# Kernel optimization log

Hardware: AMD Instinct MI355X
Metric: run time of the kernel (lower is better)

## Reference

```python
import jax, jax.numpy as jnp
import numpy as np

B, T, D, NH, L = 8192, 100, 44, 64, 8  # batch, seq/ode steps, obs_dim, rnn hidden, latent


def setup_inputs() -> dict:
    key = jax.random.key(0)
    ks = jax.random.split(key, 12)
    s = 0.1
    return {
        "x": jax.random.normal(ks[0], (B, T, D), jnp.float32),
        "mask": jax.random.randint(ks[1], (B, T, D), 0, 2).astype(jnp.float32),
        "epsilon": jax.random.normal(ks[2], (B, L), jnp.float32),
        "Wi2h": jax.random.normal(ks[3], (D + NH, NH), jnp.float32) * s,
        "bi2h": jnp.zeros((NH,), jnp.float32),
        "Wh2o": jax.random.normal(ks[4], (NH, 2 * L), jnp.float32) * s,
        "bh2o": jnp.zeros((2 * L,), jnp.float32),
        "Wf1": jax.random.normal(ks[5], (L, NH), jnp.float32) * s,
        "bf1": jnp.zeros((NH,), jnp.float32),
        "Wf2": jax.random.normal(ks[6], (NH, NH), jnp.float32) * s,
        "bf2": jnp.zeros((NH,), jnp.float32),
        "Wf3": jax.random.normal(ks[7], (NH, L), jnp.float32) * s,
        "bf3": jnp.zeros((L,), jnp.float32),
        "Wd1": jax.random.normal(ks[8], (L, NH), jnp.float32) * s,
        "bd1": jnp.zeros((NH,), jnp.float32),
        "Wd2": jax.random.normal(ks[9], (NH, D), jnp.float32) * s,
        "bd2": jnp.zeros((D,), jnp.float32),
    }


def reference(x, mask, epsilon, Wi2h, bi2h, Wh2o, bh2o,
              Wf1, bf1, Wf2, bf2, Wf3, bf3, Wd1, bd1, Wd2, bd2):
    masked_x = x * mask  # [B,T,D]

    # --- reverse-time recognition RNN (scan over time, reversed) ---
    def rnn_step(h, obs):
        h = jnp.tanh(jnp.concatenate([obs, h], axis=1) @ Wi2h + bi2h)
        return h, None

    xs_rev = jnp.transpose(masked_x[:, ::-1, :], (1, 0, 2))  # [T,B,D]
    h0 = jnp.zeros((x.shape[0], Wi2h.shape[1]), x.dtype)
    h_final, _ = jax.lax.scan(rnn_step, h0, xs_rev)
    out = h_final @ Wh2o + bh2o  # [B,2L]
    qz0_mean, qz0_logvar = out[:, :L], out[:, L:]

    # reparameterized latent sample
    z0 = epsilon * jnp.exp(0.5 * qz0_logvar) + qz0_mean  # [B,L]

    # --- latent ODE dynamics, fixed-step RK4 over ts = linspace(0,1,100) ---
    def f(z):
        h1 = jax.nn.elu(z @ Wf1 + bf1)
        h2 = jax.nn.elu(h1 @ Wf2 + bf2)
        return h2 @ Wf3 + bf3

    dt = jnp.asarray(1.0 / (T - 1), x.dtype)

    def rk4_step(z, _):
        k1 = f(z)
        k2 = f(z + 0.5 * dt * k1)
        k3 = f(z + 0.5 * dt * k2)
        k4 = f(z + dt * k3)
        zn = z + (dt / 6.0) * (k1 + 2.0 * k2 + 2.0 * k3 + k4)
        return zn, zn

    _, zs = jax.lax.scan(rk4_step, z0, None, length=T - 1)  # [T-1,B,L]
    pred_z = jnp.transpose(jnp.concatenate([z0[None], zs], axis=0), (1, 0, 2))  # [B,T,L]

    # --- decoder ---
    pred_x = jax.nn.relu(pred_z @ Wd1 + bd1) @ Wd2 + bd2  # [B,T,D]

    # fill observed entries back in
    updated_x = jnp.where(masked_x != 0, masked_x, pred_x)

    # --- loss ---
    noise_logvar = 2.0 * jnp.log(jnp.asarray(0.3, x.dtype))
    log2pi = jnp.log(jnp.asarray(2.0 * np.pi, x.dtype))
    logpx = (-0.5 * (log2pi + noise_logvar +
                     (x - updated_x) ** 2 / jnp.exp(noise_logvar))).sum((-1, -2))  # [B]
    kl = (-0.5 * qz0_logvar + (jnp.exp(qz0_logvar) + qz0_mean ** 2) / 2.0 - 0.5).sum(-1)  # [B]
    loss = jnp.mean(-logpx + kl)
    return loss
```

## Files before the change

kernel.cpp:

```cpp
#include <hip/hip_runtime.h>
#include <stdint.h>


constexpr int B_ = 8192, T_ = 100, D_ = 44, NH_ = 64, L_ = 8;

typedef __bf16 bf16x8 __attribute__((ext_vector_type(8)));
typedef float f32x4 __attribute__((ext_vector_type(4)));
typedef uint32_t u32x4 __attribute__((ext_vector_type(4)));
typedef uint32_t u32x2 __attribute__((ext_vector_type(2)));

__device__ __forceinline__ float fexp2(float x) { return __builtin_amdgcn_exp2f(x); }
__device__ __forceinline__ float frcp(float x) { return __builtin_amdgcn_rcpf(x); }
__device__ __forceinline__ float fexp(float x) { return fexp2(x * 1.44269504088896341f); }
__device__ __forceinline__ float tanh_f(float x) {
  float e = fexp2(x * 2.88539008177792681f);
  return 1.0f - 2.0f * frcp(e + 1.0f);
}
__device__ __forceinline__ float elu_f(float x) { return x > 0.0f ? x : (fexp(x) - 1.0f); }
__device__ __forceinline__ uint32_t f2bs(float x) {
  return (uint32_t)__builtin_bit_cast(unsigned short, (__bf16)x);
}
__device__ __forceinline__ uint32_t pk(float lo, float hi) { return f2bs(lo) | (f2bs(hi) << 16); }
__device__ __forceinline__ uint32_t sh(uint32_t v, int s) { return (uint32_t)__shfl((int)v, s, 64); }
__device__ __forceinline__ f32x4 mfma16(bf16x8 a, bf16x8 b, f32x4 c) {
  return __builtin_amdgcn_mfma_f32_16x16x32_bf16(a, b, c, 0, 0, 0);
}
__device__ __forceinline__ bf16x8 pack8(float a, float b, float c, float d,
                                        float e, float f, float g, float h) {
  u32x4 u = {pk(a, b), pk(c, d), pk(e, f), pk(g, h)};
  return __builtin_bit_cast(bf16x8, u);
}
__device__ __forceinline__ float f4get(const float4& f, int i) {
  return i == 0 ? f.x : (i == 1 ? f.y : (i == 2 ? f.z : f.w));
}

__device__ __forceinline__ void xbar() {
  asm volatile("s_waitcnt lgkmcnt(0)" ::: "memory");
  __builtin_amdgcn_s_barrier();
  asm volatile("" ::: "memory");
}

__device__ __forceinline__ void ex_write(uint32_t* ex, int c, int q, int w, f32x4 e) {
  u32x2 v = {pk(e[0], e[1]), pk(e[2], e[3])};
  *(u32x2*)(ex + 36 * c + 8 * w + 2 * q) = v;
}
__device__ __forceinline__ void ex_read(const uint32_t* ex, int c, int q, bf16x8* bh) {
#pragma unroll
  for (int ks = 0; ks < 2; ++ks) {
    u32x4 r = *(const u32x4*)(ex + 36 * c + 16 * ks + 4 * q);
    bh[ks] = __builtin_bit_cast(bf16x8, r);
  }
}

__device__ __forceinline__ bf16x8 build_bz(f32x4 z, int c, int q) {
  uint32_t p01 = pk(z[0], z[1]), p23 = pk(z[2], z[3]);
  u32x4 u = {sh(p01, c), sh(p23, c), sh(p01, c + 16), sh(p23, c + 16)};
  if (q == 1) u[0] = 0x3f80u;
  return __builtin_bit_cast(bf16x8, u);
}

__global__ __launch_bounds__(256) void fused_kernel(
    const float* __restrict__ x, const float* __restrict__ mask,
    const float* __restrict__ eps,
    const float* __restrict__ Wi2h, const float* __restrict__ bi2h,
    const float* __restrict__ Wh2o, const float* __restrict__ bh2o,
    const float* __restrict__ Wf1, const float* __restrict__ bf1,
    const float* __restrict__ Wf2, const float* __restrict__ bf2,
    const float* __restrict__ Wf3, const float* __restrict__ bf3,
    const float* __restrict__ Wd1, const float* __restrict__ bd1,
    const float* __restrict__ Wd2, const float* __restrict__ bd2,
    float* __restrict__ part) {
  const int tid = threadIdx.x;
  const int w = tid >> 6;
  const int lane = tid & 63;
  const int c = lane & 15, q = lane >> 4;
  const int r0 = blockIdx.x * 16;

  __shared__ __align__(16) uint32_t exA[576];
  __shared__ __align__(16) uint32_t exB[576];
  __shared__ __align__(16) uint32_t exC[576];
  __shared__ float redbuf[4];

  bf16x8 Ai[4];
#pragma unroll
  for (int ks = 0; ks < 4; ++ks) {
    bf16x8 f;
    const int m = 16 * w + c;
#pragma unroll
    for (int i = 0; i < 8; ++i) {
      const int k = 32 * ks + 8 * q + i;
      float v = 0.0f;
      if (k < 64) v = Wi2h[(44 + k) * 64 + m];
      else if (k < 108) v = Wi2h[(k - 64) * 64 + m];
      else if (k == 108) v = bi2h[m];
      f[i] = (__bf16)v;
    }
    Ai[ks] = f;
  }
  bf16x8 Ah2o[2];
#pragma unroll
  for (int ks = 0; ks < 2; ++ks) {
    bf16x8 f;
#pragma unroll
    for (int i = 0; i < 8; ++i) f[i] = (__bf16)Wh2o[(32 * ks + 8 * q + i) * 16 + c];
    Ah2o[ks] = f;
  }
  f32x4 bo;
#pragma unroll
  for (int r = 0; r < 4; ++r) bo[r] = bh2o[4 * q + r];

  const float* xrowbase = x + (size_t)(r0 + c) * T_ * D_;
  const float* mrowbase = mask + (size_t)(r0 + c) * T_ * D_;

  auto load_obs = [&](int t, float4& a0, float4& a1, float4& b0, float4& b1,
                      float4& ma0, float4& ma1, float4& mb0, float4& mb1) {
    const float4* xr = (const float4*)(xrowbase + (size_t)t * D_);
    const float4* mr = (const float4*)(mrowbase + (size_t)t * D_);
    a0 = xr[2 * q]; a1 = xr[2 * q + 1]; ma0 = mr[2 * q]; ma1 = mr[2 * q + 1];
    float4 zz = {0.f, 0.f, 0.f, 0.f};
    b0 = zz; b1 = zz; mb0 = zz; mb1 = zz;
    if (q == 0) { b0 = xr[8]; b1 = xr[9]; mb0 = mr[8]; mb1 = mr[9]; }
    else if (q == 1) { b0 = xr[10]; mb0 = mr[10]; }
  };

  f32x4 hc = {0.f, 0.f, 0.f, 0.f};
  float4 a0, a1, b0, b1, ma0, ma1, mb0, mb1;
  load_obs(T_ - 1, a0, a1, b0, b1, ma0, ma1, mb0, mb1);

#pragma unroll 1
  for (int s = 0; s < T_; ++s) {
    uint32_t* ex = (s & 1) ? exB : exA;
    ex_write(ex, c, q, w, hc);

    const int t = T_ - 1 - s;
    float4 ca0 = a0, ca1 = a1, cb0 = b0, cb1 = b1;
    float4 cm0 = ma0, cm1 = ma1, cn0 = mb0, cn1 = mb1;
    if (t > 0) load_obs(t - 1, a0, a1, b0, b1, ma0, ma1, mb0, mb1);

    bf16x8 o2 = pack8(ca0.x * cm0.x, ca0.y * cm0.y, ca0.z * cm0.z, ca0.w * cm0.w,
                      ca1.x * cm1.x, ca1.y * cm1.y, ca1.z * cm1.z, ca1.w * cm1.w);
    const float e44 = (q == 1) ? 1.0f : cb1.x * cn1.x;
    bf16x8 o3 = pack8(cb0.x * cn0.x, cb0.y * cn0.y, cb0.z * cn0.z, cb0.w * cn0.w,
                      e44, cb1.y * cn1.y, cb1.z * cn1.z, cb1.w * cn1.w);

    xbar();
    bf16x8 bh[2];
    ex_read(ex, c, q, bh);

    f32x4 zero = {0.f, 0.f, 0.f, 0.f};
    f32x4 acc = mfma16(Ai[0], bh[0], zero);
    acc = mfma16(Ai[1], bh[1], acc);
    acc = mfma16(Ai[2], o2, acc);
    acc = mfma16(Ai[3], o3, acc);
#pragma unroll
    for (int r = 0; r < 4; ++r) hc[r] = tanh_f(acc[r]);
  }

  ex_write(exA, c, q, w, hc);
  xbar();
  bf16x8 bhF[2];
  ex_read(exA, c, q, bhF);
  f32x4 o = mfma16(Ah2o[1], bhF[1], mfma16(Ah2o[0], bhF[0], bo));

  float lv[4];
#pragma unroll
  for (int r = 0; r < 4; ++r)
    lv[r] = __int_as_float(__shfl(__float_as_int(o[r]), lane + 32, 64));

  float klt = 0.0f;
  f32x4 z = {};
  if (q < 2) {
    const float4 ev = *(const float4*)(eps + (size_t)(r0 + c) * 8 + 4 * q);
#pragma unroll
    for (int r = 0; r < 4; ++r) {
      const float m = o[r];
      z[r] = f4get(ev, r) * fexp(0.5f * lv[r]) + m;
      klt += -0.5f * lv[r] + (fexp(lv[r]) + m * m) * 0.5f - 0.5f;
    }
  }
  klt += __shfl_xor(klt, 1);  klt += __shfl_xor(klt, 2);
  klt += __shfl_xor(klt, 4);  klt += __shfl_xor(klt, 8);
  klt += __shfl_xor(klt, 16); klt += __shfl_xor(klt, 32);

  __builtin_amdgcn_sched_barrier(0);

  bf16x8 A1, A2[2], A3[2], Ad1, Ad2[2];
  {
    bf16x8 f1, fd;
#pragma unroll
    for (int i = 0; i < 8; ++i) {
      const int k = 8 * q + i;
      f1[i] = (__bf16)(k < 8 ? Wf1[k * 64 + 16 * w + c] : (k == 8 ? bf1[16 * w + c] : 0.0f));
      fd[i] = (__bf16)(k < 8 ? Wd1[k * 64 + 16 * w + c] : (k == 8 ? bd1[16 * w + c] : 0.0f));
    }
    A1 = f1; Ad1 = fd;
  }
#pragma unroll
  for (int ks = 0; ks < 2; ++ks) {
    bf16x8 g;
#pragma unroll
    for (int i = 0; i < 8; ++i) g[i] = (__bf16)Wf2[(32 * ks + 8 * q + i) * 64 + 16 * w + c];
    A2[ks] = g;
  }
#pragma unroll
  for (int ks = 0; ks < 2; ++ks) {
    bf16x8 f;
#pragma unroll
    for (int i = 0; i < 8; ++i)
      f[i] = (__bf16)((c < 8) ? Wf3[(32 * ks + 8 * q + i) * 8 + c] : 0.0f);
    A3[ks] = f;
  }
#pragma unroll
  for (int ks = 0; ks < 2; ++ks) {
    bf16x8 f;
    const int m = 16 * w + c;
#pragma unroll
    for (int i = 0; i < 8; ++i)
      f[i] = (__bf16)((m < 44) ? Wd2[(32 * ks + 8 * q + i) * 44 + m] : 0.0f);
    Ad2[ks] = f;
  }
  f32x4 b2_, b3_, bd2_;
#pragma unroll
  for (int r = 0; r < 4; ++r) b2_[r] = bf2[16 * w + 4 * q + r];
#pragma unroll
  for (int r = 0; r < 4; ++r) b3_[r] = (q < 2) ? bf3[4 * q + r] : 0.0f;
#pragma unroll
  for (int r = 0; r < 4; ++r) {
    const int d = 16 * w + 4 * q + r;
    bd2_[r] = (d < 44) ? bd2[d] : 0.0f;
  }

  auto feval = [&](bf16x8 bz) -> f32x4 {
    f32x4 zero = {0.f, 0.f, 0.f, 0.f};
    f32x4 h = mfma16(A1, bz, zero);
#pragma unroll
    for (int r = 0; r < 4; ++r) h[r] = elu_f(h[r]);
    ex_write(exA, c, q, w, h);
    xbar();
    bf16x8 bh[2];
    ex_read(exA, c, q, bh);
    f32x4 g = mfma16(A2[1], bh[1], mfma16(A2[0], bh[0], b2_));
#pragma unroll
    for (int r = 0; r < 4; ++r) g[r] = elu_f(g[r]);
    ex_write(exB, c, q, w, g);
    xbar();
    bf16x8 bg[2];
    ex_read(exB, c, q, bg);
    return mfma16(A3[1], bg[1], mfma16(A3[0], bg[0], b3_));
  };

  auto load_xm = [&](int t, float4& xv, float4& mv) {
    const int d0 = 16 * w + 4 * q;
    if (w < 3 && d0 < 44) {
      const size_t off = (size_t)(r0 + c) * T_ * D_ + (size_t)t * D_ + d0;
      xv = *(const float4*)(x + off);
      mv = *(const float4*)(mask + off);
    }
  };

  const float dt = 1.0f / (float)(T_ - 1);
  const float hdt = 0.5f * dt;
  float qacc = 0.0f;

  float4 xc = {0.f, 0.f, 0.f, 0.f}, mc = xc, xn = xc, mn = xc;
  load_xm(0, xc, mc);

#pragma unroll 1
  for (int t = 0; t < T_; ++t) {
    if (t < T_ - 1) load_xm(t + 1, xn, mn);

    bf16x8 bz = build_bz(z, c, q);

    f32x4 zero = {0.f, 0.f, 0.f, 0.f};
    f32x4 hd = mfma16(Ad1, bz, zero);
#pragma unroll
    for (int r = 0; r < 4; ++r) hd[r] = fmaxf(hd[r], 0.0f);
    ex_write(exC, c, q, w, hd);
    xbar();
    if (w < 3) {
      bf16x8 bhd[2];
      ex_read(exC, c, q, bhd);
      f32x4 p = mfma16(Ad2[1], bhd[1], mfma16(Ad2[0], bhd[0], bd2_));
      if (16 * w + 4 * q < 44) {
#pragma unroll
        for (int r = 0; r < 4; ++r) {
          const float xa = f4get(xc, r), ma = f4get(mc, r);
          const float mx = xa * ma;
          const float upd = (mx != 0.0f) ? mx : p[r];
          const float df = xa - upd;
          qacc += df * df;
        }
      }
    }

    if (t < T_ - 1) {
      f32x4 k1 = feval(bz);
      f32x4 zt;
#pragma unroll
      for (int r = 0; r < 4; ++r) zt[r] = z[r] + hdt * k1[r];
      f32x4 k2 = feval(build_bz(zt, c, q));
#pragma unroll
      for (int r = 0; r < 4; ++r) zt[r] = z[r] + hdt * k2[r];
      f32x4 k3 = feval(build_bz(zt, c, q));
#pragma unroll
      for (int r = 0; r < 4; ++r) zt[r] = z[r] + dt * k3[r];
      f32x4 k4 = feval(build_bz(zt, c, q));
#pragma unroll
      for (int r = 0; r < 4; ++r)
        z[r] += (dt / 6.0f) * (k1[r] + 2.0f * (k2[r] + k3[r]) + k4[r]);
      xc = xn; mc = mn;
    }
  }

  float tot = qacc * (0.5f / 0.09f);
  tot += __shfl_xor(tot, 1);  tot += __shfl_xor(tot, 2);
  tot += __shfl_xor(tot, 4);  tot += __shfl_xor(tot, 8);
  tot += __shfl_xor(tot, 16); tot += __shfl_xor(tot, 32);
  if (lane == 0) redbuf[w] = tot;
  xbar();
  if (tid == 0)
    part[blockIdx.x] = redbuf[0] + redbuf[1] + redbuf[2] + redbuf[3] + klt;
}

__global__ __launch_bounds__(512) void reduce_kernel(const float* __restrict__ part,
                                                     float* __restrict__ out) {
  __shared__ float s[8];
  const int tid = threadIdx.x;
  float v = part[tid];
  v += __shfl_xor(v, 1);  v += __shfl_xor(v, 2);
  v += __shfl_xor(v, 4);  v += __shfl_xor(v, 8);
  v += __shfl_xor(v, 16); v += __shfl_xor(v, 32);
  if ((tid & 63) == 0) s[tid >> 6] = v;
  __syncthreads();
  if (tid == 0) {
    float acc = 0.0f;
#pragma unroll
    for (int i = 0; i < 8; ++i) acc += s[i];
    const float c0 = 0.28503427112126353f;
    out[0] = acc * (1.0f / (float)B_) - (float)(T_ * D_) * c0;
  }
}

extern "C" void kernel_launch(void* const* d_in, const int* in_sizes, int n_in,
                              void* d_out, int out_size, void* d_ws, size_t ws_size,
                              hipStream_t stream) {
  const float* x    = (const float*)d_in[0];
  const float* mask = (const float*)d_in[1];
  const float* eps  = (const float*)d_in[2];
  const float* Wi2h = (const float*)d_in[3];
  const float* bi2h = (const float*)d_in[4];
  const float* Wh2o = (const float*)d_in[5];
  const float* bh2o = (const float*)d_in[6];
  const float* Wf1  = (const float*)d_in[7];
  const float* bf1  = (const float*)d_in[8];
  const float* Wf2  = (const float*)d_in[9];
  const float* bf2  = (const float*)d_in[10];
  const float* Wf3  = (const float*)d_in[11];
  const float* bf3  = (const float*)d_in[12];
  const float* Wd1  = (const float*)d_in[13];
  const float* bd1  = (const float*)d_in[14];
  const float* Wd2  = (const float*)d_in[15];
  const float* bd2  = (const float*)d_in[16];

  float* loss = (float*)d_out;
  float* part = (float*)d_ws;

  fused_kernel<<<dim3(B_ / 16), dim3(256), 0, stream>>>(
      x, mask, eps, Wi2h, bi2h, Wh2o, bh2o, Wf1, bf1, Wf2, bf2, Wf3, bf3,
      Wd1, bd1, Wd2, bd2, part);
  reduce_kernel<<<dim3(1), dim3(512), 0, stream>>>(part, loss);
}
```

Baseline: 757.2 us.

## Compute first hidden layer redundantly per wave to drop block barriers

Each wave now computes all four 16-column tiles of the first ODE layer and the decoder's first layer itself, then repacks them through a private per-wave LDS scratch instead of a block-shared exchange. This removes one block-wide barrier per function evaluation and per decoder step, leaving one barrier per feval. exA and exB now alternate between successive fevals, which is meant to avoid write-after-read hazards without extra syncs. The cost is four times the MFMA and ELU work for layer one, more registers for A1 and Ad1, and extra LDS.

```diff
diff --git a/kernel.cpp b/kernel.cpp
--- a/kernel.cpp
+++ b/kernel.cpp
@@ -48,6 +48,20 @@
 #pragma unroll
   for (int ks = 0; ks < 2; ++ks) {
     u32x4 r = *(const u32x4*)(ex + 36 * c + 16 * ks + 4 * q);
+    bh[ks] = __builtin_bit_cast(bf16x8, r);
+  }
+}
+
+__device__ __forceinline__ void repack_lds(uint32_t* tb, int c, int q,
+                                           const f32x4* e, bf16x8* bh) {
+#pragma unroll
+  for (int tau = 0; tau < 4; ++tau) {
+    u32x2 wv = {pk(e[tau][0], e[tau][1]), pk(e[tau][2], e[tau][3])};
+    *(u32x2*)(tb + 36 * c + 8 * tau + 2 * q) = wv;
+  }
+#pragma unroll
+  for (int ks = 0; ks < 2; ++ks) {
+    u32x4 r = *(const u32x4*)(tb + 36 * c + 16 * ks + 4 * q);
     bh[ks] = __builtin_bit_cast(bf16x8, r);
   }
 }
@@ -78,8 +92,11 @@
 
   __shared__ __align__(16) uint32_t exA[576];
   __shared__ __align__(16) uint32_t exB[576];
-  __shared__ __align__(16) uint32_t exC[576];
+  __shared__ __align__(16) uint32_t tbufF[2304];
+  __shared__ __align__(16) uint32_t tbufD[2304];
   __shared__ float redbuf[4];
+  uint32_t* tbF = tbufF + 576 * w;
+  uint32_t* tbD = tbufD + 576 * w;
 
   bf16x8 Ai[4];
 #pragma unroll
@@ -184,16 +201,17 @@
 
   __builtin_amdgcn_sched_barrier(0);
 
-  bf16x8 A1, A2[2], A3[2], Ad1, Ad2[2];
-  {
+  bf16x8 A1[4], Ad1[4], A2[2], A3[2], Ad2[2];
+#pragma unroll
+  for (int tau = 0; tau < 4; ++tau) {
     bf16x8 f1, fd;
 #pragma unroll
     for (int i = 0; i < 8; ++i) {
       const int k = 8 * q + i;
-      f1[i] = (__bf16)(k < 8 ? Wf1[k * 64 + 16 * w + c] : (k == 8 ? bf1[16 * w + c] : 0.0f));
-      fd[i] = (__bf16)(k < 8 ? Wd1[k * 64 + 16 * w + c] : (k == 8 ? bd1[16 * w + c] : 0.0f));
-    }
-    A1 = f1; Ad1 = fd;
+      f1[i] = (__bf16)(k < 8 ? Wf1[k * 64 + 16 * tau + c] : (k == 8 ? bf1[16 * tau + c] : 0.0f));
+      fd[i] = (__bf16)(k < 8 ? Wd1[k * 64 + 16 * tau + c] : (k == 8 ? bd1[16 * tau + c] : 0.0f));
+    }
+    A1[tau] = f1; Ad1[tau] = fd;
   }
 #pragma unroll
   for (int ks = 0; ks < 2; ++ks) {
@@ -230,22 +248,24 @@
     bd2_[r] = (d < 44) ? bd2[d] : 0.0f;
   }
 
-  auto feval = [&](bf16x8 bz) -> f32x4 {
-    f32x4 zero = {0.f, 0.f, 0.f, 0.f};
-    f32x4 h = mfma16(A1, bz, zero);
-#pragma unroll
-    for (int r = 0; r < 4; ++r) h[r] = elu_f(h[r]);
-    ex_write(exA, c, q, w, h);
-    xbar();
+  auto feval = [&](bf16x8 bz, uint32_t* ex) -> f32x4 {
+    f32x4 h[4];
+#pragma unroll
+    for (int tau = 0; tau < 4; ++tau) {
+      f32x4 zero = {0.f, 0.f, 0.f, 0.f};
+      h[tau] = mfma16(A1[tau], bz, zero);
+#pragma unroll
+      for (int r = 0; r < 4; ++r) h[tau][r] = elu_f(h[tau][r]);
+    }
     bf16x8 bh[2];
-    ex_read(exA, c, q, bh);
+    repack_lds(tbF, c, q, h, bh);
     f32x4 g = mfma16(A2[1], bh[1], mfma16(A2[0], bh[0], b2_));
 #pragma unroll
     for (int r = 0; r < 4; ++r) g[r] = elu_f(g[r]);
-    ex_write(exB, c, q, w, g);
+    ex_write(ex, c, q, w, g);
     xbar();
     bf16x8 bg[2];
-    ex_read(exB, c, q, bg);
+    ex_read(ex, c, q, bg);
     return mfma16(A3[1], bg[1], mfma16(A3[0], bg[0], b3_));
   };
 
@@ -271,15 +291,17 @@
 
     bf16x8 bz = build_bz(z, c, q);
 
-    f32x4 zero = {0.f, 0.f, 0.f, 0.f};
-    f32x4 hd = mfma16(Ad1, bz, zero);
-#pragma unroll
-    for (int r = 0; r < 4; ++r) hd[r] = fmaxf(hd[r], 0.0f);
-    ex_write(exC, c, q, w, hd);
-    xbar();
+    f32x4 hd[4];
+#pragma unroll
+    for (int tau = 0; tau < 4; ++tau) {
+      f32x4 zero = {0.f, 0.f, 0.f, 0.f};
+      hd[tau] = mfma16(Ad1[tau], bz, zero);
+#pragma unroll
+      for (int r = 0; r < 4; ++r) hd[tau][r] = fmaxf(hd[tau][r], 0.0f);
+    }
+    bf16x8 bhd[2];
+    repack_lds(tbD, c, q, hd, bhd);
     if (w < 3) {
-      bf16x8 bhd[2];
-      ex_read(exC, c, q, bhd);
       f32x4 p = mfma16(Ad2[1], bhd[1], mfma16(Ad2[0], bhd[0], bd2_));
       if (16 * w + 4 * q < 44) {
 #pragma unroll
@@ -294,17 +316,17 @@
     }
 
     if (t < T_ - 1) {
-      f32x4 k1 = feval(bz);
+      f32x4 k1 = feval(bz, exB);
       f32x4 zt;
 #pragma unroll
       for (int r = 0; r < 4; ++r) zt[r] = z[r] + hdt * k1[r];
-      f32x4 k2 = feval(build_bz(zt, c, q));
+      f32x4 k2 = feval(build_bz(zt, c, q), exA);
 #pragma unroll
       for (int r = 0; r < 4; ++r) zt[r] = z[r] + hdt * k2[r];
-      f32x4 k3 = feval(build_bz(zt, c, q));
+      f32x4 k3 = feval(build_bz(zt, c, q), exB);
 #pragma unroll
       for (int r = 0; r < 4; ++r) zt[r] = z[r] + dt * k3[r];
-      f32x4 k4 = feval(build_bz(zt, c, q));
+      f32x4 k4 = feval(build_bz(zt, c, q), exA);
 #pragma unroll
       for (int r = 0; r < 4; ++r)
         z[r] += (dt / 6.0f) * (k1[r] + 2.0f * (k2[r] + k3[r]) + k4[r]);
```

New measurement: 917.3 us. +21.1%, slower.
